# Kernel optimization log

Measured on AMD Instinct MI355X. Metric: run time of the kernel, lower is better.

## Reference

```python
import jax, jax.numpy as jnp
import numpy as np


def setup_inputs() -> dict:
    key = jax.random.key(0)
    ks = jax.random.split(key, 12)
    B, S, H, V, T = 64, 32, 1024, 32000, 32
    s = 1.0 / np.sqrt(H)
    return {
        "encoder_outputs": jax.random.normal(ks[0], (B, S, H), jnp.float32),
        "encoder_hidden": jax.random.normal(ks[1], (1, B, H), jnp.float32),
        "input_mask": jnp.ones((B, S), dtype=bool),
        "target_tensor": jax.random.randint(ks[2], (B, T), 0, V),
        "SOS_token": 0,
        "max_len": T,
        "emb": jax.random.normal(ks[3], (V, H), jnp.float32),
        "W_ih": jax.random.uniform(ks[4], (3 * H, H), jnp.float32, -s, s),
        "W_hh": jax.random.uniform(ks[5], (3 * H, H), jnp.float32, -s, s),
        "b_ih": jax.random.uniform(ks[6], (3 * H,), jnp.float32, -s, s),
        "b_hh": jax.random.uniform(ks[7], (3 * H,), jnp.float32, -s, s),
        "out_W": jax.random.uniform(ks[8], (V, H), jnp.float32, -s, s),
        "out_b": jax.random.uniform(ks[9], (V,), jnp.float32, -s, s),
    }


def reference(encoder_outputs, encoder_hidden, input_mask, target_tensor,
              SOS_token, max_len, emb, W_ih, W_hh, b_ih, b_hh, out_W, out_b):
    B = encoder_outputs.shape[0]
    # Teacher forcing: input at step 0 is SOS, then target[:, i-1]
    tokens = jnp.concatenate(
        [jnp.full((B, 1), SOS_token, dtype=target_tensor.dtype),
         target_tensor[:, :max_len - 1]], axis=1)          # [B, T]
    # Embedding lookup + relu + input-side gate GEMM are step-independent: batch them
    x = jax.nn.relu(emb[tokens])                           # [B, T, H]
    gi = jnp.einsum('bth,gh->tbg', x, W_ih) + b_ih          # [T, B, 3H]

    def step(h, gi_t):
        gh = h @ W_hh.T + b_hh                             # [B, 3H]
        i_r, i_z, i_n = jnp.split(gi_t, 3, axis=-1)
        h_r, h_z, h_n = jnp.split(gh, 3, axis=-1)
        r = jax.nn.sigmoid(i_r + h_r)
        z = jax.nn.sigmoid(i_z + h_z)
        n = jnp.tanh(i_n + r * h_n)
        h_new = (1.0 - z) * n + z * h
        return h_new, h_new

    h0 = encoder_hidden[0]                                 # [B, H]
    h_final, hs = jax.lax.scan(step, h0, gi)               # hs: [T, B, H]
    logits = jnp.einsum('tbh,vh->btv', hs, out_W) + out_b   # [B, T, V]
    log_probs = jax.nn.log_softmax(logits, axis=-1)
    return log_probs, h_final[None]
```

## Files before the change

kernel.cpp:

```cpp
#include <hip/hip_runtime.h>
#include <hip/hip_bf16.h>
#include <math.h>

#define B_ 64
#define T_ 32
#define H_ 1024
#define V_ 32000
#define M_ (B_ * T_)
#define GRUB 64

typedef __attribute__((ext_vector_type(8))) short short8;
typedef __attribute__((ext_vector_type(4))) float f32x4;

__device__ __forceinline__ unsigned short f2bf(float f) {
  unsigned u = __float_as_uint(f);
  u = (u + 0x7FFFu + ((u >> 16) & 1u)) >> 16;
  return (unsigned short)u;
}

__device__ __forceinline__ void async16(const void* g, void* l) {
  __builtin_amdgcn_global_load_lds(
      (const __attribute__((address_space(1))) unsigned int*)g,
      (__attribute__((address_space(3))) unsigned int*)l, 16, 0, 0);
}

__global__ void k_convert(const float* __restrict__ src, short* __restrict__ dst, int n8) {
  int i = blockIdx.x * blockDim.x + threadIdx.x;
  if (i >= n8) return;
  const f32x4* s = (const f32x4*)src + (size_t)i * 2;
  f32x4 a = s[0], b = s[1];
  short8 o;
  o[0] = (short)f2bf(a[0]); o[1] = (short)f2bf(a[1]);
  o[2] = (short)f2bf(a[2]); o[3] = (short)f2bf(a[3]);
  o[4] = (short)f2bf(b[0]); o[5] = (short)f2bf(b[1]);
  o[6] = (short)f2bf(b[2]); o[7] = (short)f2bf(b[3]);
  *((short8*)dst + i) = o;
}

__global__ void k_embed(const float* __restrict__ emb, const int* __restrict__ tgt,
                        const int* __restrict__ sos, const float* __restrict__ ehid,
                        short* __restrict__ xb, short* __restrict__ hb) {
  int m = blockIdx.x, tid = threadIdx.x;
  if (m < M_) {
    int t = m >> 6, b = m & 63;
    int token = (t == 0) ? sos[0] : tgt[b * T_ + (t - 1)];
    const f32x4* s = (const f32x4*)(emb + (size_t)token * H_) + tid * 2;
    f32x4 a = s[0], c = s[1];
    short8 o;
    #pragma unroll
    for (int j = 0; j < 4; ++j) { float v = a[j] > 0.f ? a[j] : 0.f; o[j] = (short)f2bf(v); }
    #pragma unroll
    for (int j = 0; j < 4; ++j) { float v = c[j] > 0.f ? c[j] : 0.f; o[4 + j] = (short)f2bf(v); }
    *((short8*)(xb + (size_t)m * H_) + tid) = o;
  } else {
    int b = m - M_;
    const f32x4* s = (const f32x4*)(ehid + (size_t)b * H_) + tid * 2;
    f32x4 a = s[0], c = s[1];
    short8 o;
    #pragma unroll
    for (int j = 0; j < 4; ++j) o[j] = (short)f2bf(a[j]);
    #pragma unroll
    for (int j = 0; j < 4; ++j) o[4 + j] = (short)f2bf(c[j]);
    *((short8*)(hb + (size_t)b * H_) + tid) = o;
  }
}

__global__ __launch_bounds__(256, 2)
void k_gemm(const short* __restrict__ A, const short* __restrict__ Bm,
            const float* __restrict__ bias, float* __restrict__ C,
            float* __restrict__ sumexp, int N, int do_exp) {
  __shared__ short As[128 * 64];
  __shared__ short Bs[128 * 64];
  const int tid = threadIdx.x;
  const int bm = blockIdx.x, bn = blockIdx.y;
  const int w = tid >> 6, l = tid & 63;
  const int wm = (w >> 1) * 64, wn = (w & 1) * 64;
  f32x4 acc[4][4] = {};
  const short* Ab = A + (size_t)(bm * 128) * 1024;
  const short* Bb = Bm + (size_t)(bn * 128) * 1024;

  for (int kt = 0; kt < 1024; kt += 64) {
    #pragma unroll
    for (int i = 0; i < 4; ++i) {
      int g = i * 256 + tid, r = g >> 3, cp = g & 7, c = cp ^ (r & 7);
      async16(Ab + r * 1024 + kt + c * 8, &As[g * 8]);
    }
    #pragma unroll
    for (int i = 0; i < 4; ++i) {
      int g = i * 256 + tid, r = g >> 3, cp = g & 7, c = cp ^ (r & 7);
      async16(Bb + r * 1024 + kt + c * 8, &Bs[g * 8]);
    }
    __syncthreads();
    #pragma unroll
    for (int ks = 0; ks < 2; ++ks) {
      short8 af[4], bf[4];
      #pragma unroll
      for (int mi = 0; mi < 4; ++mi) {
        int row = wm + mi * 16 + (l & 15);
        int cp = (ks * 4 + (l >> 4)) ^ (row & 7);
        af[mi] = *(const short8*)&As[row * 64 + cp * 8];
      }
      #pragma unroll
      for (int ni = 0; ni < 4; ++ni) {
        int row = wn + ni * 16 + (l & 15);
        int cp = (ks * 4 + (l >> 4)) ^ (row & 7);
        bf[ni] = *(const short8*)&Bs[row * 64 + cp * 8];
      }
      #pragma unroll
      for (int mi = 0; mi < 4; ++mi)
        #pragma unroll
        for (int ni = 0; ni < 4; ++ni)
          acc[mi][ni] = __builtin_amdgcn_mfma_f32_16x16x32_bf16(af[mi], bf[ni], acc[mi][ni], 0, 0, 0);
    }
    __syncthreads();
  }

  const int row0 = bm * 128 + wm + (l >> 4) * 4;
  const int col0 = bn * 128 + wn + (l & 15);
  if (!do_exp) {
    #pragma unroll
    for (int mi = 0; mi < 4; ++mi)
      #pragma unroll
      for (int ni = 0; ni < 4; ++ni) {
        int col = col0 + ni * 16;
        float bv = bias[col];
        #pragma unroll
        for (int rg = 0; rg < 4; ++rg)
          C[(size_t)(row0 + mi * 16 + rg) * N + col] = acc[mi][ni][rg] + bv;
      }
  } else {
    #pragma unroll
    for (int mi = 0; mi < 4; ++mi) {
      float rs[4] = {0.f, 0.f, 0.f, 0.f};
      #pragma unroll
      for (int ni = 0; ni < 4; ++ni) {
        int col = col0 + ni * 16;
        float bv = bias[col];
        #pragma unroll
        for (int rg = 0; rg < 4; ++rg) {
          float v = acc[mi][ni][rg] + bv;
          C[(size_t)(row0 + mi * 16 + rg) * N + col] = v;
          rs[rg] += __expf(v);
        }
      }
      #pragma unroll
      for (int rg = 0; rg < 4; ++rg) {
        float v = rs[rg];
        #pragma unroll
        for (int off = 1; off < 16; off <<= 1) v += __shfl_xor(v, off, 64);
        if ((l & 15) == 0) atomicAdd(&sumexp[row0 + mi * 16 + rg], v);
      }
    }
  }
}

__global__ __launch_bounds__(256, 1)
void k_gru_persist(const short* __restrict__ Whh, const float* __restrict__ bhh,
                   const float* __restrict__ gi, const float* __restrict__ ehid,
                   short* __restrict__ hb0, short* __restrict__ hb1,
                   short* __restrict__ hs, float* __restrict__ hfin,
                   unsigned* __restrict__ flags) {
  __shared__ short Wlds[16 * 48 * 64];
  const int tid = threadIdx.x;
  const int bg = blockIdx.x;
  const int j0 = bg * 16;
  const int w = tid >> 6, l = tid & 63;

  #pragma unroll
  for (int i = 0; i < 24; ++i) {
    int idx = i * 256 + tid;
    int tile = idx / 384, rem = idx % 384;
    int r = rem >> 3, cp = rem & 7, c = cp ^ (r & 7);
    int gate = r >> 4, jr = r & 15;
    async16(Whh + ((size_t)(gate * 1024 + j0 + jr)) * 1024 + tile * 64 + c * 8,
            &Wlds[idx * 8]);
  }

  const int jj = j0 + (l & 15);
  const int b0 = w * 16 + (l >> 4) * 4;
  float hreg[4];
  #pragma unroll
  for (int rg = 0; rg < 4; ++rg) hreg[rg] = ehid[(size_t)(b0 + rg) * H_ + jj];
  const float bh_r = bhh[jj], bh_z = bhh[1024 + jj], bh_n = bhh[2048 + jj];

  const int arow = w * 16 + (l & 15);
  const int acol = (l >> 4) * 8;

  float gr[4], gz[4], gn[4];
  #pragma unroll
  for (int rg = 0; rg < 4; ++rg) {
    const float* gir = gi + ((size_t)(b0 + rg)) * 3072;
    gr[rg] = gir[jj];
    gz[rg] = gir[1024 + jj];
    gn[rg] = gir[2048 + jj];
  }

  __syncthreads();

  for (int t = 0; t < T_; ++t) {
    const short* hin = (t & 1) ? hb1 : hb0;
    short* hout      = (t & 1) ? hb0 : hb1;

    const short* hrow = hin + (size_t)arow * H_ + acol;
    short8 hf[32];
    #pragma unroll
    for (int ks = 0; ks < 32; ++ks)
      hf[ks] = *(const short8*)(hrow + ks * 32);

    f32x4 acc[3] = {};
    #pragma unroll
    for (int ks = 0; ks < 32; ++ks) {
      int kt64 = ks >> 1, ks2 = ks & 1;
      #pragma unroll
      for (int ga = 0; ga < 3; ++ga) {
        int brow = ga * 16 + (l & 15);
        int bcp = (ks2 * 4 + (l >> 4)) ^ (brow & 7);
        short8 bfr = *(const short8*)&Wlds[kt64 * 3072 + brow * 64 + bcp * 8];
        acc[ga] = __builtin_amdgcn_mfma_f32_16x16x32_bf16(hf[ks], bfr, acc[ga], 0, 0, 0);
      }
    }

    #pragma unroll
    for (int rg = 0; rg < 4; ++rg) {
      float r = gr[rg] + acc[0][rg] + bh_r;
      r = 1.f / (1.f + __expf(-r));
      float z = gz[rg] + acc[1][rg] + bh_z;
      z = 1.f / (1.f + __expf(-z));
      float n = tanhf(gn[rg] + r * (acc[2][rg] + bh_n));
      float hn = (1.f - z) * n + z * hreg[rg];
      hreg[rg] = hn;
      short hbv = (short)f2bf(hn);
      hout[(size_t)(b0 + rg) * H_ + jj] = hbv;
      hs[((size_t)(b0 + rg) * T_ + t) * H_ + jj] = hbv;
    }
    if (t == T_ - 1) {
      #pragma unroll
      for (int rg = 0; rg < 4; ++rg) hfin[(size_t)(b0 + rg) * H_ + jj] = hreg[rg];
      break;
    }

    __syncthreads();
    if (tid == 0) {
      __hip_atomic_store(&flags[(size_t)bg * 32], (unsigned)(t + 1),
                         __ATOMIC_RELEASE, __HIP_MEMORY_SCOPE_AGENT);
    }
    {
      #pragma unroll
      for (int rg = 0; rg < 4; ++rg) {
        const float* gir = gi + ((size_t)((t + 1) * 64) + b0 + rg) * 3072;
        gr[rg] = gir[jj];
        gz[rg] = gir[1024 + jj];
        gn[rg] = gir[2048 + jj];
      }
    }
    if (w == 0) {
      const unsigned tgt = (unsigned)(t + 1);
      while (true) {
        unsigned v = __hip_atomic_load(&flags[(size_t)l * 32],
                                       __ATOMIC_RELAXED, __HIP_MEMORY_SCOPE_AGENT);
        if (__all(v >= tgt)) break;
      }
    }
    __syncthreads();
    __builtin_amdgcn_fence(__ATOMIC_ACQUIRE, "agent");
  }
}

__global__ void k_lse(float* s) {
  int i = blockIdx.x * 256 + threadIdx.x;
  if (i < M_) s[i] = logf(s[i]);
}

__global__ void k_sub(float* __restrict__ out, const float* __restrict__ lse) {
  size_t vid = (size_t)blockIdx.x * 256 + threadIdx.x;
  int r = (int)(vid / (V_ / 4));
  float ls = lse[r];
  f32x4* p = (f32x4*)out + vid;
  f32x4 v = *p;
  v[0] -= ls; v[1] -= ls; v[2] -= ls; v[3] -= ls;
  *p = v;
}

extern "C" void kernel_launch(void* const* d_in, const int* in_sizes, int n_in,
                              void* d_out, int out_size, void* d_ws, size_t ws_size,
                              hipStream_t stream) {
  const float* ehid = (const float*)d_in[1];
  const int*   tgt  = (const int*)d_in[3];
  const int*   sos  = (const int*)d_in[4];
  const float* emb  = (const float*)d_in[6];
  const float* Wih  = (const float*)d_in[7];
  const float* Whh  = (const float*)d_in[8];
  const float* bih  = (const float*)d_in[9];
  const float* bhh  = (const float*)d_in[10];
  const float* outW = (const float*)d_in[11];
  const float* outb = (const float*)d_in[12];
  float* out = (float*)d_out;

  char* ws = (char*)d_ws;
  size_t off = 0;
  auto alloc = [&](size_t bytes) -> void* {
    void* p = ws + off;
    off = (off + bytes + 255) & ~(size_t)255;
    return p;
  };
  short* outW_b = (short*)alloc((size_t)V_ * H_ * 2);
  short* Wih_b  = (short*)alloc((size_t)3 * H_ * H_ * 2);
  short* Whh_b  = (short*)alloc((size_t)3 * H_ * H_ * 2);
  short* xb     = (short*)alloc((size_t)M_ * H_ * 2);
  float* gi     = (float*)alloc((size_t)M_ * 3 * H_ * 4);
  short* hs     = (short*)alloc((size_t)M_ * H_ * 2);
  short* hb0    = (short*)alloc((size_t)B_ * H_ * 2);
  short* hb1    = (short*)alloc((size_t)B_ * H_ * 2);
  float* sume   = (float*)alloc((size_t)M_ * 4);
  unsigned* flags = (unsigned*)alloc(GRUB * 32 * 4);

  k_convert<<<V_ * H_ / 8 / 256, 256, 0, stream>>>(outW, outW_b, V_ * H_ / 8);
  k_convert<<<3 * H_ * H_ / 8 / 256, 256, 0, stream>>>(Wih, Wih_b, 3 * H_ * H_ / 8);
  k_convert<<<3 * H_ * H_ / 8 / 256, 256, 0, stream>>>(Whh, Whh_b, 3 * H_ * H_ / 8);

  hipMemsetAsync(flags, 0, GRUB * 32 * 4, stream);
  hipMemsetAsync(sume, 0, M_ * 4, stream);

  k_embed<<<M_ + B_, 128, 0, stream>>>(emb, tgt, sos, ehid, xb, hb0);

  dim3 g1(M_ / 128, 3 * H_ / 128);
  k_gemm<<<g1, 256, 0, stream>>>(xb, Wih_b, bih, gi, nullptr, 3 * H_, 0);

  k_gru_persist<<<GRUB, 256, 0, stream>>>(Whh_b, bhh, gi, ehid, hb0, hb1, hs,
                                          out + (size_t)B_ * T_ * V_, flags);

  dim3 g2(M_ / 128, V_ / 128);
  k_gemm<<<g2, 256, 0, stream>>>(hs, outW_b, outb, out, sume, V_, 1);

  k_lse<<<8, 256, 0, stream>>>(sume);
  k_sub<<<(int)((size_t)B_ * T_ * V_ / 4 / 256), 256, 0, stream>>>(out, sume);
}
```

Before: 1.027 ms.

## Split GRU recurrence over K across waves with register-resident W_hh slices

The persistent GRU kernel now has each wave own a quarter of the K dimension. Each wave keeps its W_hh fragments in registers for the whole run and computes partial products for all 64 batch rows. The partials are then reduced through LDS, which reuses the weight buffer. This replaces the per-step full-K LDS weight reads and the 32-deep h load per wave with fewer h loads per lane. It also swaps the release/acquire atomics and fences for inline-asm sc0 sc1 cache-bypassing loads and stores plus explicit waitcnt, which cuts synchronization cost but relies on hardware coherence semantics and risks memory-ordering correctness.

```diff
diff --git a/kernel.cpp b/kernel.cpp
--- a/kernel.cpp
+++ b/kernel.cpp
@@ -161,6 +161,7 @@
                    short* __restrict__ hs, float* __restrict__ hfin,
                    unsigned* __restrict__ flags) {
   __shared__ short Wlds[16 * 48 * 64];
+  float* red = (float*)Wlds;
   const int tid = threadIdx.x;
   const int bg = blockIdx.x;
   const int j0 = bg * 16;
@@ -183,9 +184,6 @@
   for (int rg = 0; rg < 4; ++rg) hreg[rg] = ehid[(size_t)(b0 + rg) * H_ + jj];
   const float bh_r = bhh[jj], bh_z = bhh[1024 + jj], bh_n = bhh[2048 + jj];
 
-  const int arow = w * 16 + (l & 15);
-  const int acol = (l >> 4) * 8;
-
   float gr[4], gz[4], gn[4];
   #pragma unroll
   for (int rg = 0; rg < 4; ++rg) {
@@ -197,41 +195,85 @@
 
   __syncthreads();
 
+  short8 wreg[3][8];
+  #pragma unroll
+  for (int ks = 0; ks < 8; ++ks) {
+    int kt64 = w * 4 + (ks >> 1), ks2 = ks & 1;
+    #pragma unroll
+    for (int ga = 0; ga < 3; ++ga) {
+      int brow = ga * 16 + (l & 15);
+      int bcp = (ks2 * 4 + (l >> 4)) ^ (brow & 7);
+      wreg[ga][ks] = *(const short8*)&Wlds[kt64 * 3072 + brow * 64 + bcp * 8];
+    }
+  }
+  __syncthreads();
+
+  size_t aoff[4];
+  #pragma unroll
+  for (int mi = 0; mi < 4; ++mi)
+    aoff[mi] = (size_t)(mi * 16 + (l & 15)) * H_ + w * 256 + (l >> 4) * 8;
+
   for (int t = 0; t < T_; ++t) {
     const short* hin = (t & 1) ? hb1 : hb0;
     short* hout      = (t & 1) ? hb0 : hb1;
 
-    const short* hrow = hin + (size_t)arow * H_ + acol;
-    short8 hf[32];
-    #pragma unroll
-    for (int ks = 0; ks < 32; ++ks)
-      hf[ks] = *(const short8*)(hrow + ks * 32);
-
-    f32x4 acc[3] = {};
-    #pragma unroll
-    for (int ks = 0; ks < 32; ++ks) {
-      int kt64 = ks >> 1, ks2 = ks & 1;
-      #pragma unroll
-      for (int ga = 0; ga < 3; ++ga) {
-        int brow = ga * 16 + (l & 15);
-        int bcp = (ks2 * 4 + (l >> 4)) ^ (brow & 7);
-        short8 bfr = *(const short8*)&Wlds[kt64 * 3072 + brow * 64 + bcp * 8];
-        acc[ga] = __builtin_amdgcn_mfma_f32_16x16x32_bf16(hf[ks], bfr, acc[ga], 0, 0, 0);
+    short8 hf[4][8];
+    #pragma unroll
+    for (int mi = 0; mi < 4; ++mi)
+      #pragma unroll
+      for (int ks = 0; ks < 8; ++ks) {
+        const short* hp = hin + aoff[mi] + ks * 32;
+        asm volatile("global_load_dwordx4 %0, %1, off sc0 sc1"
+                     : "=v"(hf[mi][ks]) : "v"(hp) : "memory");
+      }
+    asm volatile("s_waitcnt vmcnt(0)" ::: "memory");
+    __builtin_amdgcn_sched_barrier(0);
+
+    f32x4 acc[4][3] = {};
+    #pragma unroll
+    for (int ks = 0; ks < 8; ++ks)
+      #pragma unroll
+      for (int mi = 0; mi < 4; ++mi)
+        #pragma unroll
+        for (int ga = 0; ga < 3; ++ga)
+          acc[mi][ga] = __builtin_amdgcn_mfma_f32_16x16x32_bf16(
+              hf[mi][ks], wreg[ga][ks], acc[mi][ga], 0, 0, 0);
+
+    #pragma unroll
+    for (int mi = 0; mi < 4; ++mi) {
+      if (mi == w) continue;
+      #pragma unroll
+      for (int ga = 0; ga < 3; ++ga)
+        *(f32x4*)&red[((size_t)(w * 12 + mi * 3 + ga)) * 256 + l * 4] = acc[mi][ga];
+    }
+    __syncthreads();
+    f32x4 tot[3];
+    #pragma unroll
+    for (int ga = 0; ga < 3; ++ga) {
+      tot[ga] = acc[w][ga];
+      #pragma unroll
+      for (int sw = 0; sw < 4; ++sw) {
+        if (sw == w) continue;
+        f32x4 p = *(const f32x4*)&red[((size_t)(sw * 12 + w * 3 + ga)) * 256 + l * 4];
+        tot[ga][0] += p[0]; tot[ga][1] += p[1];
+        tot[ga][2] += p[2]; tot[ga][3] += p[3];
       }
     }
 
     #pragma unroll
     for (int rg = 0; rg < 4; ++rg) {
-      float r = gr[rg] + acc[0][rg] + bh_r;
+      float r = gr[rg] + tot[0][rg] + bh_r;
       r = 1.f / (1.f + __expf(-r));
-      float z = gz[rg] + acc[1][rg] + bh_z;
+      float z = gz[rg] + tot[1][rg] + bh_z;
       z = 1.f / (1.f + __expf(-z));
-      float n = tanhf(gn[rg] + r * (acc[2][rg] + bh_n));
+      float n = tanhf(gn[rg] + r * (tot[2][rg] + bh_n));
       float hn = (1.f - z) * n + z * hreg[rg];
       hreg[rg] = hn;
-      short hbv = (short)f2bf(hn);
-      hout[(size_t)(b0 + rg) * H_ + jj] = hbv;
-      hs[((size_t)(b0 + rg) * T_ + t) * H_ + jj] = hbv;
+      unsigned hbv = (unsigned)f2bf(hn);
+      const short* hp = hout + (size_t)(b0 + rg) * H_ + jj;
+      asm volatile("global_store_short %0, %1, off sc0 sc1"
+                   :: "v"(hp), "v"(hbv) : "memory");
+      hs[((size_t)(b0 + rg) * T_ + t) * H_ + jj] = (short)hbv;
     }
     if (t == T_ - 1) {
       #pragma unroll
@@ -239,19 +281,20 @@
       break;
     }
 
+    asm volatile("s_waitcnt vmcnt(0)" ::: "memory");
     __syncthreads();
     if (tid == 0) {
-      __hip_atomic_store(&flags[(size_t)bg * 32], (unsigned)(t + 1),
-                         __ATOMIC_RELEASE, __HIP_MEMORY_SCOPE_AGENT);
-    }
-    {
-      #pragma unroll
-      for (int rg = 0; rg < 4; ++rg) {
-        const float* gir = gi + ((size_t)((t + 1) * 64) + b0 + rg) * 3072;
-        gr[rg] = gir[jj];
-        gz[rg] = gir[1024 + jj];
-        gn[rg] = gir[2048 + jj];
-      }
+      unsigned val = (unsigned)(t + 1);
+      const unsigned* fp = &flags[(size_t)bg * 32];
+      asm volatile("global_store_dword %0, %1, off sc0 sc1"
+                   :: "v"(fp), "v"(val) : "memory");
+    }
+    #pragma unroll
+    for (int rg = 0; rg < 4; ++rg) {
+      const float* gir = gi + ((size_t)((t + 1) * 64) + b0 + rg) * 3072;
+      gr[rg] = gir[jj];
+      gz[rg] = gir[1024 + jj];
+      gn[rg] = gir[2048 + jj];
     }
     if (w == 0) {
       const unsigned tgt = (unsigned)(t + 1);
@@ -262,7 +305,6 @@
       }
     }
     __syncthreads();
-    __builtin_amdgcn_fence(__ATOMIC_ACQUIRE, "agent");
   }
 }
 
```

Result: faster. 949.6 us (-7.5%).
